# Performance work log

Hardware: AMD Instinct MI355X
Metric: run time of the kernel (lower is better)

## Reference

```python
import jax, jax.numpy as jnp
import numpy as np

B, S, D = 2, 2048, 2048
QH, KVH, HD = 32, 8, 64
GROUPS = QH // KVH
EPS = 1e-6


def rms_norm(x, w):
    # normalize over last dim (head_dim)
    var = jnp.mean(x * x, axis=-1, keepdims=True)
    return x * jax.lax.rsqrt(var + EPS) * w


def apply_rope(x, freq):
    # x: (b,h,s,hd); freq: (1,1,s,hd//2) angles; interleaved-pair rotation
    xr = x.reshape(*x.shape[:-1], HD // 2, 2)
    x1, x2 = xr[..., 0], xr[..., 1]
    cos, sin = jnp.cos(freq), jnp.sin(freq)
    o1 = x1 * cos - x2 * sin
    o2 = x1 * sin + x2 * cos
    return jnp.stack([o1, o2], axis=-1).reshape(x.shape)


def setup_inputs() -> dict:
    key = jax.random.key(0)
    ks = jax.random.split(key, 8)
    x = jax.random.normal(ks[0], (B, S, D), dtype=jnp.float32)
    freq = jax.random.normal(ks[1], (1, 1, S, HD // 2), dtype=jnp.float32)
    w = 0.02
    wq = jax.random.normal(ks[2], (QH * HD, D), dtype=jnp.float32) * w
    wk = jax.random.normal(ks[3], (KVH * HD, D), dtype=jnp.float32) * w
    wv = jax.random.normal(ks[4], (KVH * HD, D), dtype=jnp.float32) * w
    wo = jax.random.normal(ks[5], (D, QH * HD), dtype=jnp.float32) * w
    q_norm_w = jnp.ones((HD,), dtype=jnp.float32)
    k_norm_w = jnp.ones((HD,), dtype=jnp.float32)
    return {"x": x, "freq": freq, "wq": wq, "wk": wk, "wv": wv,
            "wo": wo, "q_norm_w": q_norm_w, "k_norm_w": k_norm_w}


def reference(x, freq, wq, wk, wv, wo, q_norm_w, k_norm_w):
    b, s, d = x.shape
    scale = HD ** -0.5
    q = (x @ wq.T).reshape(b, s, QH, HD).transpose(0, 2, 1, 3)   # (b,QH,s,hd)
    k = (x @ wk.T).reshape(b, s, KVH, HD).transpose(0, 2, 1, 3)  # (b,KVH,s,hd)
    v = (x @ wv.T).reshape(b, s, KVH, HD).transpose(0, 2, 1, 3)
    q = rms_norm(q, q_norm_w)
    k = rms_norm(k, k_norm_w)
    q = apply_rope(q, freq)
    k = apply_rope(k, freq)
    k_new, v_new = k, v
    # GQA: group q-heads per kv-head instead of repeat_interleave on k/v
    qg = q.reshape(b, KVH, GROUPS, s, HD)
    scores = jnp.einsum('bkgqd,bktd->bkgqt', qg, k) * scale
    causal = jnp.triu(jnp.ones((s, s), dtype=bool), k=1)
    scores = jnp.where(causal, -jnp.inf, scores)
    p = jax.nn.softmax(scores, axis=-1)
    o = jnp.einsum('bkgqt,bktd->bkgqd', p, v)
    o = o.reshape(b, QH, s, HD).transpose(0, 2, 1, 3).reshape(b, s, QH * HD)
    return (o @ wo.T, k_new, v_new)
```

## Files before the change

kernel.cpp:

```cpp
#include <hip/hip_runtime.h>
#include <hip/hip_bf16.h>
#include <stdint.h>


#define B_  2
#define S_  2048
#define D_  2048
#define QH_ 32
#define KVH_ 8
#define HD_ 64

typedef unsigned short u16;
typedef __bf16  bf16x8 __attribute__((ext_vector_type(8)));
typedef float   f32x4  __attribute__((ext_vector_type(4)));
typedef u16     u16x8  __attribute__((ext_vector_type(8)));

__device__ __forceinline__ u16 f2b(float f) {
  unsigned u = __float_as_uint(f);
  u += 0x7fffu + ((u >> 16) & 1u);
  return (u16)(u >> 16);
}

__device__ __forceinline__ void gload16(const void* g, void* l) {
  __builtin_amdgcn_global_load_lds(
      (const __attribute__((address_space(1))) void*)(uintptr_t)g,
      (__attribute__((address_space(3))) void*)(uint32_t)(uintptr_t)l,
      16, 0, 0);
}

#define LDS8(buf, row, g) \
  (*reinterpret_cast<const bf16x8*>(&(buf)[(row) * 64 + ((((g) ^ ((row) & 7))) << 3)]))

__global__ __launch_bounds__(256) void cast_f32_bf16(
    const float* __restrict__ in, u16* __restrict__ out, int n4) {
  int i = blockIdx.x * 256 + threadIdx.x;
  if (i >= n4) return;
  float4 v = *reinterpret_cast<const float4*>(&in[(size_t)i * 4]);
  u16 o0 = f2b(v.x), o1 = f2b(v.y), o2 = f2b(v.z), o3 = f2b(v.w);
  unsigned lo = (unsigned)o0 | ((unsigned)o1 << 16);
  unsigned hi = (unsigned)o2 | ((unsigned)o3 << 16);
  uint2 pk; pk.x = lo; pk.y = hi;
  *reinterpret_cast<uint2*>(&out[(size_t)i * 4]) = pk;
}

__global__ __launch_bounds__(512) void gemm_bt(
    const u16* __restrict__ A, const u16* __restrict__ Bm,
    float* __restrict__ C, int M, int N, int K) {
  __shared__ u16 lA[128 * 64];
  __shared__ u16 lB[128 * 64];
  const int t = threadIdx.x, lane = t & 63, wid = t >> 6;
  const int nwg = gridDim.x * gridDim.y;
  const int flat = blockIdx.y * gridDim.x + blockIdx.x;
  const int swz = (flat & 7) * (nwg >> 3) + (flat >> 3);
  const int m0 = (swz / gridDim.x) * 128, n0 = (swz % gridDim.x) * 128;
  const int wr = wid >> 1, wc = wid & 1;
  f32x4 acc[2][4] = {};
  const int srow = t >> 3;
  const int sg8 = (((t & 7) ^ (srow & 7)) << 3);
  const u16* gA = A + (size_t)(m0 + srow) * K + sg8;
  const u16* gB = Bm + (size_t)(n0 + srow) * K + sg8;
  const int rb = lane & 15, hi = lane >> 4;

  for (int k0 = 0; k0 < K; k0 += 64) {
    gload16(gA + k0,                  &lA[wid * 512]);
    gload16(gA + k0 + (size_t)64 * K, &lA[4096 + wid * 512]);
    gload16(gB + k0,                  &lB[wid * 512]);
    gload16(gB + k0 + (size_t)64 * K, &lB[4096 + wid * 512]);
    __syncthreads();
#pragma unroll
    for (int half = 0; half < 2; half++) {
      bf16x8 af[2], bfr[4];
#pragma unroll
      for (int i = 0; i < 2; i++)
        af[i] = LDS8(lA, wr * 32 + i * 16 + rb, half * 4 + hi);
#pragma unroll
      for (int j = 0; j < 4; j++)
        bfr[j] = LDS8(lB, wc * 64 + j * 16 + rb, half * 4 + hi);
#pragma unroll
      for (int i = 0; i < 2; i++)
#pragma unroll
        for (int j = 0; j < 4; j++)
          acc[i][j] = __builtin_amdgcn_mfma_f32_16x16x32_bf16(af[i], bfr[j], acc[i][j], 0, 0, 0);
    }
    __syncthreads();
  }
  const int rg = hi * 4;
#pragma unroll
  for (int i = 0; i < 2; i++)
#pragma unroll
    for (int j = 0; j < 4; j++)
#pragma unroll
      for (int r = 0; r < 4; r++)
        C[(size_t)(m0 + wr * 32 + i * 16 + rg + r) * N + (n0 + wc * 64 + j * 16 + rb)] = acc[i][j][r];
}

__global__ __launch_bounds__(256) void postproc(
    const float* __restrict__ lin, const float* __restrict__ freq,
    const float* __restrict__ nw, u16* __restrict__ outb,
    float* __restrict__ outf, int H, float oscale) {
  int p = blockIdx.x * 256 + threadIdx.x;
  int i = p & 31;
  int h = (p >> 5) & (H - 1);
  int s = (p / (32 * H)) & (S_ - 1);
  int b = p / (32 * H * S_);
  float2 xv = *reinterpret_cast<const float2*>(
      &lin[(((size_t)b * S_ + s) * H + h) * 64 + 2 * i]);
  float x1 = xv.x, x2 = xv.y;
  float ss = x1 * x1 + x2 * x2;
  ss += __shfl_xor(ss, 1);  ss += __shfl_xor(ss, 2);
  ss += __shfl_xor(ss, 4);  ss += __shfl_xor(ss, 8);
  ss += __shfl_xor(ss, 16);
  float inv = rsqrtf(ss * (1.0f / 64.0f) + 1e-6f);
  x1 *= inv * nw[2 * i];
  x2 *= inv * nw[2 * i + 1];
  float a = freq[(size_t)s * 32 + i];
  float sn, cs;
  __sincosf(a, &sn, &cs);
  float o1 = (x1 * cs - x2 * sn) * oscale;
  float o2 = (x1 * sn + x2 * cs) * oscale;
  size_t oidx = (((size_t)b * H + h) * S_ + s) * 64 + 2 * i;
  unsigned pk = (unsigned)f2b(o1) | ((unsigned)f2b(o2) << 16);
  *reinterpret_cast<unsigned*>(&outb[oidx]) = pk;
  if (outf) {
    float2 o; o.x = o1; o.y = o2;
    *reinterpret_cast<float2*>(&outf[oidx]) = o;
  }
}

__global__ __launch_bounds__(256) void v_trans(
    const float* __restrict__ vlin, float* __restrict__ vnew,
    u16* __restrict__ vtb) {
  __shared__ u16 tile[64 * 72];
  const int blk = blockIdx.x;
  const int st = blk & 31, kvh = (blk >> 5) & 7, b = blk >> 8;
  const int t = threadIdx.x;
  const int sl = t >> 2, c0 = (t & 3) * 16;
  const size_t src  = (((size_t)b * S_ + st * 64 + sl) * KVH_ + kvh) * 64 + c0;
  const size_t dstf = (((size_t)(b * KVH_ + kvh) * S_) + st * 64 + sl) * 64 + c0;
#pragma unroll
  for (int i = 0; i < 4; i++) {
    float4 f = *reinterpret_cast<const float4*>(&vlin[src + i * 4]);
    *reinterpret_cast<float4*>(&vnew[dstf + i * 4]) = f;
    tile[(c0 + i * 4 + 0) * 72 + sl] = f2b(f.x);
    tile[(c0 + i * 4 + 1) * 72 + sl] = f2b(f.y);
    tile[(c0 + i * 4 + 2) * 72 + sl] = f2b(f.z);
    tile[(c0 + i * 4 + 3) * 72 + sl] = f2b(f.w);
  }
  __syncthreads();
  const int hd = t >> 2, p0 = (t & 3) * 16;
  const size_t dstt = ((size_t)(b * KVH_ + kvh) * 64 + hd) * S_ + st * 64 + p0;
  uint4 lo = *reinterpret_cast<const uint4*>(&tile[hd * 72 + p0]);
  uint4 hi = *reinterpret_cast<const uint4*>(&tile[hd * 72 + p0 + 8]);
  *reinterpret_cast<uint4*>(&vtb[dstt])     = lo;
  *reinterpret_cast<uint4*>(&vtb[dstt + 8]) = hi;
}

__global__ __launch_bounds__(256, 4) void attn_fwd(
    const u16* __restrict__ Qb, const u16* __restrict__ Kb,
    const u16* __restrict__ Vt, u16* __restrict__ Ob) {
  __shared__ u16 lQ[4096];
  __shared__ u16 lK[2][4096];
  __shared__ u16 lV[2][4096];

  const int t = threadIdx.x, lane = t & 63, wid = t >> 6;
  const int blk = blockIdx.x;
  const int qt = 31 - (blk >> 6);
  const int bh = blk & 63;
  const int h = bh & 31;
  const int b = bh >> 5;
  const int kvh = h >> 2;
  const int q0 = qt * 64;
  const size_t qbase  = ((size_t)(b * QH_ + h) * S_ + q0) * 64;
  const size_t kbase  = ((size_t)(b * KVH_ + kvh) * S_) * 64;
  const size_t vtbase = ((size_t)(b * KVH_ + kvh) * 64) * S_;

  const int srow = t >> 3;
  const int sg8 = (((t & 7) ^ (srow & 7)) << 3);

  {
    gload16(Qb + qbase + (size_t)srow * 64 + sg8,        &lQ[wid * 512]);
    gload16(Qb + qbase + (size_t)(32 + srow) * 64 + sg8, &lQ[2048 + wid * 512]);
  }
#define STAGE_KV(kdst, vdst, t0)                                              \
  {                                                                           \
    gload16(Kb + kbase + (size_t)((t0) + srow) * 64 + sg8,      &(kdst)[wid * 512]); \
    gload16(Kb + kbase + (size_t)((t0) + 32 + srow) * 64 + sg8, &(kdst)[2048 + wid * 512]); \
    gload16(Vt + vtbase + (size_t)srow * S_ + (t0) + sg8,        &(vdst)[wid * 512]); \
    gload16(Vt + vtbase + (size_t)(32 + srow) * S_ + (t0) + sg8, &(vdst)[2048 + wid * 512]); \
  }
  STAGE_KV(lK[0], lV[0], 0)
  __syncthreads();

  const int rb = lane & 15, hi = lane >> 4;
  const bf16x8 aq0 = LDS8(lQ, wid * 16 + rb, hi);
  const bf16x8 aq1 = LDS8(lQ, wid * 16 + rb, 4 + hi);
  u16* lPw = &lQ[wid * 1024];

  f32x4 accO[4] = {};
  float M[4], L[4];
#pragma unroll
  for (int r = 0; r < 4; r++) { M[r] = -1e30f; L[r] = 0.0f; }

  const int nt = qt + 1;
  for (int tt = 0; tt < nt; ++tt) {
    const int cur = tt & 1;
    if (tt + 1 < nt) STAGE_KV(lK[cur ^ 1], lV[cur ^ 1], (tt + 1) * 64)
    const u16* lKc = lK[cur];
    const u16* lVc = lV[cur];

    f32x4 sc[4] = {};
#pragma unroll
    for (int nf = 0; nf < 4; nf++) {
      bf16x8 b0 = LDS8(lKc, nf * 16 + rb, hi);
      bf16x8 b1 = LDS8(lKc, nf * 16 + rb, 4 + hi);
      sc[nf] = __builtin_amdgcn_mfma_f32_16x16x32_bf16(aq0, b0, sc[nf], 0, 0, 0);
      sc[nf] = __builtin_amdgcn_mfma_f32_16x16x32_bf16(aq1, b1, sc[nf], 0, 0, 0);
    }
    if (tt == qt) {
      const int t0 = tt * 64;
#pragma unroll
      for (int nf = 0; nf < 4; nf++) {
        int colg = t0 + nf * 16 + rb;
#pragma unroll
        for (int r = 0; r < 4; r++) {
          int rowg = q0 + wid * 16 + hi * 4 + r;
          if (colg > rowg) sc[nf][r] = -1e30f;
        }
      }
    }
    float fac[4];
#pragma unroll
    for (int r = 0; r < 4; r++) {
      float mx = fmaxf(fmaxf(sc[0][r], sc[1][r]), fmaxf(sc[2][r], sc[3][r]));
      mx = fmaxf(mx, __shfl_xor(mx, 1));
      mx = fmaxf(mx, __shfl_xor(mx, 2));
      mx = fmaxf(mx, __shfl_xor(mx, 4));
      mx = fmaxf(mx, __shfl_xor(mx, 8));
      float mn = fmaxf(M[r], mx);
      fac[r] = exp2f(M[r] - mn);
      M[r] = mn;
    }
    float rs[4] = {0.f, 0.f, 0.f, 0.f};
#pragma unroll
    for (int nf = 0; nf < 4; nf++)
#pragma unroll
      for (int r = 0; r < 4; r++) {
        float pv = exp2f(sc[nf][r] - M[r]);
        sc[nf][r] = pv;
        rs[r] += pv;
      }
#pragma unroll
    for (int r = 0; r < 4; r++) {
      float s4 = rs[r];
      s4 += __shfl_xor(s4, 1); s4 += __shfl_xor(s4, 2);
      s4 += __shfl_xor(s4, 4); s4 += __shfl_xor(s4, 8);
      L[r] = L[r] * fac[r] + s4;
      accO[0][r] *= fac[r]; accO[1][r] *= fac[r];
      accO[2][r] *= fac[r]; accO[3][r] *= fac[r];
    }
#pragma unroll
    for (int nf = 0; nf < 4; nf++)
#pragma unroll
      for (int r = 0; r < 4; r++) {
        float own = sc[nf][r];
        float oth = __shfl_xor(own, 1);
        if (!(lane & 1)) {
          int row = hi * 4 + r;
          int col = nf * 16 + rb;
          unsigned pk = (unsigned)f2b(own) | ((unsigned)f2b(oth) << 16);
          *reinterpret_cast<unsigned*>(&lPw[row * 64 + (col ^ ((row & 7) << 3))]) = pk;
        }
      }
#pragma unroll
    for (int ks = 0; ks < 2; ks++) {
      bf16x8 ap = LDS8(lPw, rb, ks * 4 + hi);
#pragma unroll
      for (int nf = 0; nf < 4; nf++) {
        bf16x8 bv = LDS8(lVc, nf * 16 + rb, ks * 4 + hi);
        accO[nf] = __builtin_amdgcn_mfma_f32_16x16x32_bf16(ap, bv, accO[nf], 0, 0, 0);
      }
    }
    __syncthreads();
  }
  float inv[4];
#pragma unroll
  for (int r = 0; r < 4; r++) inv[r] = 1.0f / L[r];
#pragma unroll
  for (int nf = 0; nf < 4; nf++)
#pragma unroll
    for (int r = 0; r < 4; r++) {
      float own = accO[nf][r] * inv[r];
      float oth = __shfl_xor(own, 1);
      if (!(lane & 1)) {
        int rowg = q0 + wid * 16 + hi * 4 + r;
        size_t idx = ((size_t)b * S_ + rowg) * (QH_ * HD_) + h * 64 + nf * 16 + rb;
        unsigned pk = (unsigned)f2b(own) | ((unsigned)f2b(oth) << 16);
        *reinterpret_cast<unsigned*>(&Ob[idx]) = pk;
      }
    }
}

extern "C" void kernel_launch(void* const* d_in, const int* in_sizes, int n_in,
                              void* d_out, int out_size, void* d_ws, size_t ws_size,
                              hipStream_t stream) {
  const float* x    = (const float*)d_in[0];
  const float* freq = (const float*)d_in[1];
  const float* wq   = (const float*)d_in[2];
  const float* wk   = (const float*)d_in[3];
  const float* wv   = (const float*)d_in[4];
  const float* wo   = (const float*)d_in[5];
  const float* qnw  = (const float*)d_in[6];
  const float* knw  = (const float*)d_in[7];
  float* out = (float*)d_out;

  char* ws = (char*)d_ws;
  u16*  xb   = (u16*)(ws);
  u16*  wqb  = (u16*)(ws + 16777216);
  u16*  wkb  = (u16*)(ws + 25165824);
  u16*  wvb  = (u16*)(ws + 27262976);
  float* qlin = (float*)(ws + 29360128);
  float* klin = (float*)(ws + 62914560);
  float* vlin = (float*)(ws + 71303168);
  u16*  qb   = (u16*)(ws + 79691776);
  u16*  kb   = (u16*)(ws + 96468992);
  u16*  vtb  = (u16*)(ws + 100663296);
  u16*  wob = wqb;
  u16*  ob  = (u16*)qlin;

  cast_f32_bf16<<<8192, 256, 0, stream>>>(x, xb, 2097152);
  cast_f32_bf16<<<4096, 256, 0, stream>>>(wq, wqb, 1048576);
  cast_f32_bf16<<<1024, 256, 0, stream>>>(wk, wkb, 262144);
  cast_f32_bf16<<<1024, 256, 0, stream>>>(wv, wvb, 262144);
  dim3 gq(16, 32), gkv(4, 32);
  gemm_bt<<<gq, 512, 0, stream>>>(xb, wqb, qlin, 4096, 2048, 2048);
  gemm_bt<<<gkv, 512, 0, stream>>>(xb, wkb, klin, 4096, 512, 2048);
  gemm_bt<<<gkv, 512, 0, stream>>>(xb, wvb, vlin, 4096, 512, 2048);
  postproc<<<16384, 256, 0, stream>>>(qlin, freq, qnw, qb, nullptr, QH_, 0.18033688011112042f);
  postproc<<<4096, 256, 0, stream>>>(klin, freq, knw, kb, out + 8388608, KVH_, 1.0f);
  v_trans<<<512, 256, 0, stream>>>(vlin, out + 10485760, vtb);
  cast_f32_bf16<<<4096, 256, 0, stream>>>(wo, wob, 1048576);
  attn_fwd<<<2048, 256, 0, stream>>>(qb, kb, vtb, ob);
  gemm_bt<<<gq, 512, 0, stream>>>(ob, wob, out, 4096, 2048, 2048);
}
```

Before: 438.2 us.

## Defer softmax row-sum reduction, write P without shuffles, change LDS swizzle

The attention kernel now keeps per-lane partial row sums and does the cross-lane shuffle reduction once at the end instead of on every KV tile. P is written to LDS as individual bf16 stores rather than shuffling pairs and having half the lanes do packed stores. The LDS XOR swizzle is changed to also mix in row>>3, applied to both the GEMM and attention tiles, to reduce bank conflicts for the new store pattern. The cost is more, narrower LDS store instructions in exchange for fewer cross-lane shuffles in the inner loop.

```diff
diff --git a/kernel.cpp b/kernel.cpp
--- a/kernel.cpp
+++ b/kernel.cpp
@@ -28,8 +28,10 @@
       16, 0, 0);
 }
 
+#define SWZK(row) ((((row) ^ (((row) >> 3) << 1))) & 7)
+
 #define LDS8(buf, row, g) \
-  (*reinterpret_cast<const bf16x8*>(&(buf)[(row) * 64 + ((((g) ^ ((row) & 7))) << 3)]))
+  (*reinterpret_cast<const bf16x8*>(&(buf)[(row) * 64 + (((g) ^ SWZK(row)) << 3)]))
 
 __global__ __launch_bounds__(256) void cast_f32_bf16(
     const float* __restrict__ in, u16* __restrict__ out, int n4) {
@@ -56,7 +58,7 @@
   const int wr = wid >> 1, wc = wid & 1;
   f32x4 acc[2][4] = {};
   const int srow = t >> 3;
-  const int sg8 = (((t & 7) ^ (srow & 7)) << 3);
+  const int sg8 = (((t & 7) ^ SWZK(srow)) << 3);
   const u16* gA = A + (size_t)(m0 + srow) * K + sg8;
   const u16* gB = Bm + (size_t)(n0 + srow) * K + sg8;
   const int rb = lane & 15, hi = lane >> 4;
@@ -175,7 +177,7 @@
   const size_t vtbase = ((size_t)(b * KVH_ + kvh) * 64) * S_;
 
   const int srow = t >> 3;
-  const int sg8 = (((t & 7) ^ (srow & 7)) << 3);
+  const int sg8 = (((t & 7) ^ SWZK(srow)) << 3);
 
   {
     gload16(Qb + qbase + (size_t)srow * 64 + sg8,        &lQ[wid * 512]);
@@ -197,9 +199,9 @@
   u16* lPw = &lQ[wid * 1024];
 
   f32x4 accO[4] = {};
-  float M[4], L[4];
-#pragma unroll
-  for (int r = 0; r < 4; r++) { M[r] = -1e30f; L[r] = 0.0f; }
+  float M[4], Lp[4];
+#pragma unroll
+  for (int r = 0; r < 4; r++) { M[r] = -1e30f; Lp[r] = 0.0f; }
 
   const int nt = qt + 1;
   for (int tt = 0; tt < nt; ++tt) {
@@ -240,37 +242,28 @@
       fac[r] = exp2f(M[r] - mn);
       M[r] = mn;
     }
-    float rs[4] = {0.f, 0.f, 0.f, 0.f};
-#pragma unroll
-    for (int nf = 0; nf < 4; nf++)
-#pragma unroll
-      for (int r = 0; r < 4; r++) {
+#pragma unroll
+    for (int r = 0; r < 4; r++) {
+      float rs = 0.f;
+#pragma unroll
+      for (int nf = 0; nf < 4; nf++) {
         float pv = exp2f(sc[nf][r] - M[r]);
         sc[nf][r] = pv;
-        rs[r] += pv;
-      }
-#pragma unroll
-    for (int r = 0; r < 4; r++) {
-      float s4 = rs[r];
-      s4 += __shfl_xor(s4, 1); s4 += __shfl_xor(s4, 2);
-      s4 += __shfl_xor(s4, 4); s4 += __shfl_xor(s4, 8);
-      L[r] = L[r] * fac[r] + s4;
+        rs += pv;
+      }
+      Lp[r] = Lp[r] * fac[r] + rs;
       accO[0][r] *= fac[r]; accO[1][r] *= fac[r];
       accO[2][r] *= fac[r]; accO[3][r] *= fac[r];
     }
 #pragma unroll
-    for (int nf = 0; nf < 4; nf++)
+    for (int nf = 0; nf < 4; nf++) {
+      const int cg = nf * 2 + (rb >> 3), co = rb & 7;
 #pragma unroll
       for (int r = 0; r < 4; r++) {
-        float own = sc[nf][r];
-        float oth = __shfl_xor(own, 1);
-        if (!(lane & 1)) {
-          int row = hi * 4 + r;
-          int col = nf * 16 + rb;
-          unsigned pk = (unsigned)f2b(own) | ((unsigned)f2b(oth) << 16);
-          *reinterpret_cast<unsigned*>(&lPw[row * 64 + (col ^ ((row & 7) << 3))]) = pk;
-        }
-      }
+        int row = hi * 4 + r;
+        lPw[row * 64 + ((cg ^ SWZK(row)) << 3) + co] = f2b(sc[nf][r]);
+      }
+    }
 #pragma unroll
     for (int ks = 0; ks < 2; ks++) {
       bf16x8 ap = LDS8(lPw, rb, ks * 4 + hi);
@@ -284,7 +277,12 @@
   }
   float inv[4];
 #pragma unroll
-  for (int r = 0; r < 4; r++) inv[r] = 1.0f / L[r];
+  for (int r = 0; r < 4; r++) {
+    float Ls = Lp[r];
+    Ls += __shfl_xor(Ls, 1); Ls += __shfl_xor(Ls, 2);
+    Ls += __shfl_xor(Ls, 4); Ls += __shfl_xor(Ls, 8);
+    inv[r] = 1.0f / Ls;
+  }
 #pragma unroll
   for (int nf = 0; nf < 4; nf++)
 #pragma unroll
```

Result: faster. 407.0 us (-7.1%).
